# Optimization experiments

Measured on AMD Instinct MI355X. Metric: run time of the kernel, lower is better.

## Reference

```python
import jax, jax.numpy as jnp
import numpy as np

NUM_HEADS = 8
NUM_LEVELS = 4
NUM_POINTS = 4
EMBED = 256
HEAD_DIM = EMBED // NUM_HEADS
SPATIAL = [(100, 100), (50, 50), (25, 25), (13, 13)]  # (H, W) per level


def _bilinear_sample(val, grid):
    """torch.nn.functional.grid_sample(mode='bilinear', padding_mode='zeros', align_corners=False).
    val: [B, H, W, C], grid: [B, N, 2] with (x, y) in [-1, 1]. Returns [B, N, C]."""
    B, H, W, C = val.shape
    x = (grid[..., 0] + 1.0) * (W * 0.5) - 0.5
    y = (grid[..., 1] + 1.0) * (H * 0.5) - 0.5
    x0 = jnp.floor(x)
    y0 = jnp.floor(y)
    wx1 = x - x0
    wy1 = y - y0
    wx0 = 1.0 - wx1
    wy0 = 1.0 - wy1
    x0i = x0.astype(jnp.int32)
    y0i = y0.astype(jnp.int32)
    valf = val.reshape(B, H * W, C)

    def corner(xi, yi, w):
        valid = (xi >= 0) & (xi < W) & (yi >= 0) & (yi < H)
        idx = jnp.clip(yi, 0, H - 1) * W + jnp.clip(xi, 0, W - 1)
        v = jnp.take_along_axis(valf, idx[..., None], axis=1)  # [B, N, C]
        return v * (w * valid)[..., None]

    return (corner(x0i, y0i, wx0 * wy0) + corner(x0i + 1, y0i, wx1 * wy0)
            + corner(x0i, y0i + 1, wx0 * wy1) + corner(x0i + 1, y0i + 1, wx1 * wy1))


def setup_inputs() -> dict:
    key = jax.random.key(0)
    ks = jax.random.split(key, 12)
    bs, nq = 4, 6000
    nv = sum(h * w for h, w in SPATIAL)
    s = 0.02
    return {
        "query": jax.random.normal(ks[0], (bs, nq, EMBED), jnp.float32),
        "value": jax.random.normal(ks[1], (bs, nv, EMBED), jnp.float32),
        "reference_points": jax.random.uniform(ks[2], (bs, nq, NUM_LEVELS, 2), jnp.float32),
        "W_off": jax.random.normal(ks[3], (EMBED, NUM_HEADS * NUM_LEVELS * NUM_POINTS * 2), jnp.float32) * s,
        "b_off": jax.random.normal(ks[4], (NUM_HEADS * NUM_LEVELS * NUM_POINTS * 2,), jnp.float32),
        "W_attn": jax.random.normal(ks[5], (EMBED, NUM_HEADS * NUM_LEVELS * NUM_POINTS), jnp.float32) * s,
        "b_attn": jnp.zeros((NUM_HEADS * NUM_LEVELS * NUM_POINTS,), jnp.float32),
        "W_val": jax.random.normal(ks[6], (EMBED, EMBED), jnp.float32) * s,
        "b_val": jnp.zeros((EMBED,), jnp.float32),
        "W_out": jax.random.normal(ks[7], (EMBED, EMBED), jnp.float32) * s,
        "b_out": jnp.zeros((EMBED,), jnp.float32),
        "spatial_shapes": jnp.asarray(np.array(SPATIAL, dtype=np.int32)),
    }


def reference(query, value, reference_points, W_off, b_off, W_attn, b_attn,
              W_val, b_val, W_out, b_out, spatial_shapes):
    shapes = [(int(h), int(w)) for h, w in np.asarray(spatial_shapes)]
    bs, nq, _ = query.shape
    nv = value.shape[1]

    v = (value @ W_val + b_val).reshape(bs, nv, NUM_HEADS, HEAD_DIM)
    offsets = (query @ W_off + b_off).reshape(bs, nq, NUM_HEADS, NUM_LEVELS, NUM_POINTS, 2)
    aw = (query @ W_attn + b_attn).reshape(bs, nq, NUM_HEADS, NUM_LEVELS * NUM_POINTS)
    aw = jax.nn.softmax(aw, axis=-1).reshape(bs, nq, NUM_HEADS, NUM_LEVELS, NUM_POINTS)

    # offset normalizer is [W, H] per level
    norm = jnp.asarray([[w, h] for h, w in shapes], dtype=query.dtype)  # [L, 2]
    loc = reference_points[:, :, None, :, None, :] + offsets / norm[None, None, None, :, None, :]
    grids = 2.0 * loc - 1.0  # [bs, nq, H, L, P, 2]
    # -> [bs*H, nq*P, 2] per level
    grids = jnp.transpose(grids, (0, 2, 1, 3, 4, 5)).reshape(bs * NUM_HEADS, nq, NUM_LEVELS, NUM_POINTS, 2)

    v_bh = jnp.transpose(v, (0, 2, 1, 3)).reshape(bs * NUM_HEADS, nv, HEAD_DIM)
    sampled = []
    start = 0
    for l, (H_, W_) in enumerate(shapes):
        val_l = v_bh[:, start:start + H_ * W_].reshape(bs * NUM_HEADS, H_, W_, HEAD_DIM)
        grid_l = grids[:, :, l].reshape(bs * NUM_HEADS, nq * NUM_POINTS, 2)
        s_l = _bilinear_sample(val_l, grid_l).reshape(bs * NUM_HEADS, nq, NUM_POINTS, HEAD_DIM)
        sampled.append(s_l)
        start += H_ * W_
    sampled = jnp.stack(sampled, axis=2)  # [bs*H, nq, L, P, c]

    aw_bh = jnp.transpose(aw, (0, 2, 1, 3, 4)).reshape(bs * NUM_HEADS, nq, NUM_LEVELS, NUM_POINTS)
    out = (sampled * aw_bh[..., None]).sum(axis=(2, 3))  # [bs*H, nq, c]
    out = out.reshape(bs, NUM_HEADS, nq, HEAD_DIM).transpose(0, 2, 1, 3).reshape(bs, nq, EMBED)
    out = out @ W_out + b_out
    return out + query
```

## Files before the change

kernel.cpp:

```cpp
#include <hip/hip_runtime.h>
#include <hip/hip_bf16.h>

#define BS 4
#define NQ 6000
#define NV 13294
#define NH 8
#define HD 32
#define EMB 256
#define MV (BS * NV)
#define MQ (BS * NQ)

typedef __attribute__((ext_vector_type(8))) short short8;
typedef __attribute__((ext_vector_type(4))) float floatx4;

__device__ __constant__ float LVL_DIM[4] = {100.f, 50.f, 25.f, 13.f};

__device__ inline unsigned short bf16bits(float f) {
  __hip_bfloat16 h = __float2bfloat16(f);
  return *reinterpret_cast<unsigned short*>(&h);
}
__device__ inline float bflo(unsigned int u) { return __uint_as_float(u << 16); }
__device__ inline float bfhi(unsigned int u) { return __uint_as_float(u & 0xffff0000u); }

#define LDSTR 72

__global__ __launch_bounds__(256) void wtrans_kernel(
    const float* __restrict__ W_val, const float* __restrict__ W_off,
    const float* __restrict__ W_attn, const float* __restrict__ W_out,
    unsigned short* __restrict__ Wt_val, unsigned short* __restrict__ Wt_qcat,
    unsigned short* __restrict__ Wt_out) {
  const int b = blockIdx.x, k = threadIdx.x;
  if (b < 256) {
    Wt_val[b * EMB + k] = bf16bits(W_val[k * 256 + b]);
  } else if (b < 640) {
    const int n = b - 256;
    float v = (n < 256) ? W_off[k * 256 + n] : W_attn[k * 128 + (n - 256)];
    Wt_qcat[n * EMB + k] = bf16bits(v);
  } else {
    const int n = b - 640;
    Wt_out[n * EMB + k] = bf16bits(W_out[k * 256 + n]);
  }
}

__device__ inline void loadA_f32(const float* __restrict__ A, int M, int m0,
                                 int k0, int tid, float4 ra[8]) {
  const int r = tid >> 1, half = tid & 1;
  const int row = m0 + r;
  if (row < M) {
    const float* src = A + (size_t)row * EMB + k0 + half * 32;
#pragma unroll
    for (int j = 0; j < 8; ++j) ra[j] = *(const float4*)(src + 4 * j);
  } else {
#pragma unroll
    for (int j = 0; j < 8; ++j) ra[j] = make_float4(0.f, 0.f, 0.f, 0.f);
  }
}
__device__ inline void storeA_lds(unsigned short* lds, int tid,
                                  const float4 ra[8]) {
  const int r = tid >> 1, half = tid & 1;
  unsigned short* dst = lds + r * LDSTR + half * 32;
#pragma unroll
  for (int j = 0; j < 8; ++j) {
    ushort4 u;
    u.x = bf16bits(ra[j].x);
    u.y = bf16bits(ra[j].y);
    u.z = bf16bits(ra[j].z);
    u.w = bf16bits(ra[j].w);
    *(ushort4*)(dst + 4 * j) = u;
  }
}
__device__ inline void loadB_bf16(const unsigned short* __restrict__ B, int M,
                                  int n0, int k0, int tid, uint4 rb[4]) {
  const int r = tid >> 1, half = tid & 1;
  const int row = n0 + r;
  if (row < M) {
    const unsigned short* src = B + (size_t)row * EMB + k0 + half * 32;
#pragma unroll
    for (int j = 0; j < 4; ++j) rb[j] = *(const uint4*)(src + 8 * j);
  } else {
#pragma unroll
    for (int j = 0; j < 4; ++j) rb[j] = make_uint4(0, 0, 0, 0);
  }
}
__device__ inline void storeB_lds(unsigned short* lds, int tid,
                                  const uint4 rb[4]) {
  const int r = tid >> 1, half = tid & 1;
  unsigned short* dst = lds + r * LDSTR + half * 32;
#pragma unroll
  for (int j = 0; j < 4; ++j) *(uint4*)(dst + 8 * j) = rb[j];
}

__device__ inline void mfma_step(const unsigned short* ldsA,
                                 const unsigned short* ldsB, int wm, int wn,
                                 int lane, int ksub, floatx4 acc[4][4]) {
  const unsigned short* ap =
      ldsA + (wm * 64 + (lane & 15)) * LDSTR + ksub + (lane >> 4) * 8;
  const unsigned short* bp =
      ldsB + (wn * 64 + (lane & 15)) * LDSTR + ksub + (lane >> 4) * 8;
  short8 af[4], bfr[4];
#pragma unroll
  for (int t = 0; t < 4; ++t) {
    af[t] = *(const short8*)(ap + t * 16 * LDSTR);
    bfr[t] = *(const short8*)(bp + t * 16 * LDSTR);
  }
#pragma unroll
  for (int mt = 0; mt < 4; ++mt)
#pragma unroll
    for (int nt = 0; nt < 4; ++nt)
      acc[mt][nt] = __builtin_amdgcn_mfma_f32_16x16x32_bf16(af[mt], bfr[nt],
                                                            acc[mt][nt], 0, 0, 0);
}

__device__ inline void gemm_loop_f32A(const float* __restrict__ A, int M,
                                      int m0, const unsigned short* __restrict__ B,
                                      int NB, int n0, unsigned short* ldsA,
                                      unsigned short* ldsB, int tid, int wm,
                                      int wn, int lane, floatx4 acc[4][4]) {
  float4 ra[8];
  uint4 rb[4];
  loadA_f32(A, M, m0, 0, tid, ra);
  loadB_bf16(B, NB, n0, 0, tid, rb);
#pragma unroll
  for (int k = 0; k < 4; ++k) {
    storeA_lds(ldsA, tid, ra);
    storeB_lds(ldsB, tid, rb);
    __syncthreads();
    if (k < 3) {
      loadA_f32(A, M, m0, (k + 1) * 64, tid, ra);
      loadB_bf16(B, NB, n0, (k + 1) * 64, tid, rb);
    }
    mfma_step(ldsA, ldsB, wm, wn, lane, 0, acc);
    mfma_step(ldsA, ldsB, wm, wn, lane, 32, acc);
    __syncthreads();
  }
}

__device__ inline void gemm_loop_bf16A(const unsigned short* __restrict__ A,
                                       int M, int m0,
                                       const unsigned short* __restrict__ B,
                                       int NB, int n0, unsigned short* ldsA,
                                       unsigned short* ldsB, int tid, int wm,
                                       int wn, int lane, floatx4 acc[4][4]) {
  uint4 ra[4], rb[4];
  loadB_bf16(A, M, m0, 0, tid, ra);
  loadB_bf16(B, NB, n0, 0, tid, rb);
#pragma unroll
  for (int k = 0; k < 4; ++k) {
    storeB_lds(ldsA, tid, ra);
    storeB_lds(ldsB, tid, rb);
    __syncthreads();
    if (k < 3) {
      loadB_bf16(A, M, m0, (k + 1) * 64, tid, ra);
      loadB_bf16(B, NB, n0, (k + 1) * 64, tid, rb);
    }
    mfma_step(ldsA, ldsB, wm, wn, lane, 0, acc);
    mfma_step(ldsA, ldsB, wm, wn, lane, 32, acc);
    __syncthreads();
  }
}

__global__ __launch_bounds__(256, 2) void vqproj_kernel(
    const float* __restrict__ value, const unsigned short* __restrict__ Wt_val,
    const float* __restrict__ b_val, unsigned short* __restrict__ vbh,
    const float* __restrict__ query, const unsigned short* __restrict__ Wt_qcat,
    const float* __restrict__ refpts, const float* __restrict__ b_off,
    const float* __restrict__ b_attn, float* __restrict__ locbuf,
    float* __restrict__ awbuf) {
  __shared__ unsigned short ldsA[128 * LDSTR];
  __shared__ unsigned short ldsB[128 * LDSTR];
  const int tid = threadIdx.x, lane = tid & 63, w = tid >> 6;
  const int wm = w >> 1, wn = w & 1;
  floatx4 acc[4][4];
  const floatx4 zero = {0.f, 0.f, 0.f, 0.f};
#pragma unroll
  for (int i2 = 0; i2 < 4; i2++)
#pragma unroll
    for (int j = 0; j < 4; j++) acc[i2][j] = zero;
  const int quad = lane >> 4, cl = lane & 15;

  if (blockIdx.x < 832) {
    const int chunk = blockIdx.x >> 4, i = blockIdx.x & 15;
    const int m0 = (chunk * 8 + (i & 7)) * 128;
    const int n0 = (i >> 3) * 128;
    gemm_loop_f32A(value, MV, m0, Wt_val, 256, n0, ldsA, ldsB, tid, wm, wn,
                   lane, acc);
#pragma unroll
    for (int mt = 0; mt < 4; ++mt) {
#pragma unroll
      for (int r = 0; r < 4; ++r) {
        const int row = m0 + wm * 64 + mt * 16 + quad * 4 + r;
        if (row < MV) {
          const int b = row / NV, n = row - b * NV;
#pragma unroll
          for (int nt = 0; nt < 4; ++nt) {
            const int c = n0 + wn * 64 + nt * 16 + cl;
            const int h = c >> 5, d = c & 31;
            vbh[(((size_t)(b * NH + h)) * NV + n) * HD + d] =
                bf16bits(acc[mt][nt][r] + b_val[c]);
          }
        }
      }
    }
  } else {
    const int bid = blockIdx.x - 832;
    const int chunk = bid / 24, i = bid % 24;
    const int m_idx = chunk * 8 + (i & 7);
    if (m_idx >= 188) return;
    const int m0 = m_idx * 128;
    const int n0 = (i >> 3) * 128;
    gemm_loop_f32A(query, MQ, m0, Wt_qcat, 384, n0, ldsA, ldsB, tid, wm, wn,
                   lane, acc);
    if (n0 < 256) {
#pragma unroll
      for (int mt = 0; mt < 4; ++mt) {
#pragma unroll
        for (int r = 0; r < 4; ++r) {
          const int row = m0 + wm * 64 + mt * 16 + quad * 4 + r;
          if (row < MQ) {
#pragma unroll
            for (int nt = 0; nt < 4; ++nt) {
              const int c = n0 + wn * 64 + nt * 16 + cl;
              const int xy = c & 1, l = (c >> 3) & 3;
              const float dim = LVL_DIM[l];
              const float ref = refpts[(size_t)row * 8 + l * 2 + xy];
              locbuf[(size_t)row * 256 + c] =
                  ref * dim + acc[mt][nt][r] + b_off[c] - 0.5f;
            }
          }
        }
      }
    } else {
#pragma unroll
      for (int mt = 0; mt < 4; ++mt) {
#pragma unroll
        for (int r = 0; r < 4; ++r) {
          const int row = m0 + wm * 64 + mt * 16 + quad * 4 + r;
          if (row < MQ) {
#pragma unroll
            for (int nt = 0; nt < 4; ++nt) {
              const int ca = wn * 64 + nt * 16 + cl;
              float v = acc[mt][nt][r] + b_attn[ca];
              float m = v;
              m = fmaxf(m, __shfl_xor(m, 1));
              m = fmaxf(m, __shfl_xor(m, 2));
              m = fmaxf(m, __shfl_xor(m, 4));
              m = fmaxf(m, __shfl_xor(m, 8));
              float e = __expf(v - m);
              float s = e;
              s += __shfl_xor(s, 1);
              s += __shfl_xor(s, 2);
              s += __shfl_xor(s, 4);
              s += __shfl_xor(s, 8);
              awbuf[(size_t)row * 128 + ca] = e / s;
            }
          }
        }
      }
    }
  }
}

__global__ __launch_bounds__(256, 4) void sample_kernel(
    const unsigned short* __restrict__ vbh, const float* __restrict__ locbuf,
    const float* __restrict__ awbuf, unsigned short* __restrict__ sampledb) {
  const int blk = blockIdx.x;
  const int t = blk >> 3;
  const int quarter = t / 750;
  const int j = t - quarter * 750;
  const int slice = (blk & 7) * 4 + quarter;
  const int h = slice & 7;
  const int w = threadIdx.x >> 6;
  const int lane = threadIdx.x & 63;
  const int r0 = (slice >> 3) * NQ + j * 8 + w * 2;
  const int g = lane >> 2;
  const int d8 = lane & 3;
  const int l = g >> 2;

  const int W_ = (l < 2) ? ((l == 0) ? 100 : 50) : ((l == 2) ? 25 : 13);
  const int START = (l < 2) ? ((l == 0) ? 0 : 10000) : ((l == 2) ? 12500 : 13125);
  const unsigned int* base =
      (const unsigned int*)vbh + ((size_t)slice * NV + START) * 16 + d8 * 4;

  float acc0[8], acc1[8];
#pragma unroll
  for (int rr = 0; rr < 2; ++rr) {
    const int row = r0 + rr;
    float* a = rr ? acc1 : acc0;
    const float2 xy =
        *(const float2*)(locbuf + (size_t)row * 256 + h * 32 + g * 2);
    const float wgt = awbuf[(size_t)row * 128 + h * 16 + g];

    const float fx = floorf(xy.x), fy = floorf(xy.y);
    const int x0 = (int)fx, y0 = (int)fy;
    const float wx1 = xy.x - fx, wy1 = xy.y - fy;
    const float wx0 = 1.f - wx1, wy0 = 1.f - wy1;
    const int x0c = min(max(x0, 0), W_ - 1), x1c = min(max(x0 + 1, 0), W_ - 1);
    const int y0c = min(max(y0, 0), W_ - 1), y1c = min(max(y0 + 1, 0), W_ - 1);
    const float mx0 = ((unsigned)x0 < (unsigned)W_) ? wx0 : 0.f;
    const float mx1 = ((unsigned)(x0 + 1) < (unsigned)W_) ? wx1 : 0.f;
    const float my0 = ((unsigned)y0 < (unsigned)W_) ? wy0 : 0.f;
    const float my1 = ((unsigned)(y0 + 1) < (unsigned)W_) ? wy1 : 0.f;
    const float wy0w = wgt * my0, wy1w = wgt * my1;
    const float w00 = wy0w * mx0, w01 = wy0w * mx1;
    const float w10 = wy1w * mx0, w11 = wy1w * mx1;

    const int rb0 = y0c * W_, rb1 = y1c * W_;
    const uint4 u00 = *(const uint4*)(base + (size_t)(rb0 + x0c) * 16);
    const uint4 u01 = *(const uint4*)(base + (size_t)(rb0 + x1c) * 16);
    const uint4 u10 = *(const uint4*)(base + (size_t)(rb1 + x0c) * 16);
    const uint4 u11 = *(const uint4*)(base + (size_t)(rb1 + x1c) * 16);
    const unsigned int* p00 = &u00.x;
    const unsigned int* p01 = &u01.x;
    const unsigned int* p10 = &u10.x;
    const unsigned int* p11 = &u11.x;
#pragma unroll
    for (int k = 0; k < 4; ++k) {
      a[2 * k] = w00 * bflo(p00[k]) + w01 * bflo(p01[k]) + w10 * bflo(p10[k]) +
                 w11 * bflo(p11[k]);
      a[2 * k + 1] = w00 * bfhi(p00[k]) + w01 * bfhi(p01[k]) +
                     w10 * bfhi(p10[k]) + w11 * bfhi(p11[k]);
    }
  }

  const bool b0 = (lane >> 2) & 1;
  const bool b1 = (lane >> 3) & 1;
  const bool b2 = (lane >> 4) & 1;
#pragma unroll
  for (int rr = 0; rr < 2; ++rr) {
    float* v = rr ? acc1 : acc0;
#pragma unroll
    for (int jj = 0; jj < 4; ++jj) {
      float lo = v[jj], hi = v[jj + 4];
      float recv = __shfl_xor(b0 ? lo : hi, 4);
      v[jj] = (b0 ? hi : lo) + recv;
    }
#pragma unroll
    for (int jj = 0; jj < 2; ++jj) {
      float lo = v[jj], hi = v[jj + 2];
      float recv = __shfl_xor(b1 ? lo : hi, 8);
      v[jj] = (b1 ? hi : lo) + recv;
    }
    {
      float lo = v[0], hi = v[1];
      float recv = __shfl_xor(b2 ? lo : hi, 16);
      v[0] = (b2 ? hi : lo) + recv;
    }
    v[0] += __shfl_xor(v[0], 32);
  }

  const int dim = d8 * 8 + (b0 ? 4 : 0) + (b1 ? 2 : 0) + (b2 ? 1 : 0);
  const int row = (lane < 32) ? r0 : (r0 + 1);
  const float val = (lane < 32) ? acc0[0] : acc1[0];
  sampledb[(size_t)row * EMB + h * 32 + dim] = bf16bits(val);
}

__global__ __launch_bounds__(256, 2) void oproj_kernel(
    const unsigned short* __restrict__ sampledb,
    const unsigned short* __restrict__ Wt, const float* __restrict__ b_out,
    const float* __restrict__ query, float* __restrict__ out) {
  __shared__ unsigned short ldsA[128 * LDSTR];
  __shared__ unsigned short ldsB[128 * LDSTR];
  const int tid = threadIdx.x, lane = tid & 63, w = tid >> 6;
  const int wm = w >> 1, wn = w & 1;
  const int chunk = blockIdx.x >> 4, i = blockIdx.x & 15;
  const int m_idx = chunk * 8 + (i & 7);
  if (m_idx >= 188) return;
  const int m0 = m_idx * 128;
  const int n0 = (i >> 3) * 128;
  floatx4 acc[4][4];
  const floatx4 zero = {0.f, 0.f, 0.f, 0.f};
#pragma unroll
  for (int i2 = 0; i2 < 4; i2++)
#pragma unroll
    for (int j = 0; j < 4; j++) acc[i2][j] = zero;

  gemm_loop_bf16A(sampledb, MQ, m0, Wt, 256, n0, ldsA, ldsB, tid, wm, wn, lane,
                  acc);

  const int quad = lane >> 4, cl = lane & 15;
#pragma unroll
  for (int mt = 0; mt < 4; ++mt) {
#pragma unroll
    for (int r = 0; r < 4; ++r) {
      const int row = m0 + wm * 64 + mt * 16 + quad * 4 + r;
      if (row < MQ) {
#pragma unroll
        for (int nt = 0; nt < 4; ++nt) {
          const int c = n0 + wn * 64 + nt * 16 + cl;
          out[(size_t)row * EMB + c] =
              acc[mt][nt][r] + b_out[c] + query[(size_t)row * EMB + c];
        }
      }
    }
  }
}

extern "C" void kernel_launch(void* const* d_in, const int* in_sizes, int n_in,
                              void* d_out, int out_size, void* d_ws,
                              size_t ws_size, hipStream_t stream) {
  const float* query  = (const float*)d_in[0];
  const float* value  = (const float*)d_in[1];
  const float* refpts = (const float*)d_in[2];
  const float* W_off  = (const float*)d_in[3];
  const float* b_off  = (const float*)d_in[4];
  const float* W_attn = (const float*)d_in[5];
  const float* b_attn = (const float*)d_in[6];
  const float* W_val  = (const float*)d_in[7];
  const float* b_val  = (const float*)d_in[8];
  const float* W_out  = (const float*)d_in[9];
  const float* b_out  = (const float*)d_in[10];
  float* out = (float*)d_out;

  char* ws = (char*)d_ws;
  unsigned short* vbh = (unsigned short*)ws;
  float* locbuf = (float*)(ws + 27226112);
  float* awbuf = (float*)(ws + 51802112);
  unsigned short* sampledb = (unsigned short*)(ws + 64090112);
  unsigned short* Wt_val = (unsigned short*)(ws + 76378112);
  unsigned short* Wt_qcat = (unsigned short*)(ws + 76509184);
  unsigned short* Wt_out = (unsigned short*)(ws + 76705792);

  wtrans_kernel<<<896, 256, 0, stream>>>(W_val, W_off, W_attn, W_out, Wt_val,
                                         Wt_qcat, Wt_out);
  vqproj_kernel<<<1408, 256, 0, stream>>>(value, Wt_val, b_val, vbh, query,
                                          Wt_qcat, refpts, b_off, b_attn,
                                          locbuf, awbuf);
  sample_kernel<<<24000, 256, 0, stream>>>(vbh, locbuf, awbuf, sampledb);
  oproj_kernel<<<384, 256, 0, stream>>>(sampledb, Wt_out, b_out, query, out);
}
```

Measured before the change: 247.7 us.

## Keep full weight tile resident in LDS and stream A directly into registers

```diff
diff --git a/kernel.cpp b/kernel.cpp
--- a/kernel.cpp
+++ b/kernel.cpp
@@ -22,7 +22,18 @@
 __device__ inline float bflo(unsigned int u) { return __uint_as_float(u << 16); }
 __device__ inline float bfhi(unsigned int u) { return __uint_as_float(u & 0xffff0000u); }
 
-#define LDSTR 72
+__device__ inline short8 cvt8(float4 a, float4 b) {
+  short8 r;
+  r[0] = (short)bf16bits(a.x);
+  r[1] = (short)bf16bits(a.y);
+  r[2] = (short)bf16bits(a.z);
+  r[3] = (short)bf16bits(a.w);
+  r[4] = (short)bf16bits(b.x);
+  r[5] = (short)bf16bits(b.y);
+  r[6] = (short)bf16bits(b.z);
+  r[7] = (short)bf16bits(b.w);
+  return r;
+}
 
 __global__ __launch_bounds__(256) void wtrans_kernel(
     const float* __restrict__ W_val, const float* __restrict__ W_off,
@@ -42,120 +53,119 @@
   }
 }
 
-__device__ inline void loadA_f32(const float* __restrict__ A, int M, int m0,
-                                 int k0, int tid, float4 ra[8]) {
-  const int r = tid >> 1, half = tid & 1;
-  const int row = m0 + r;
-  if (row < M) {
-    const float* src = A + (size_t)row * EMB + k0 + half * 32;
-#pragma unroll
-    for (int j = 0; j < 8; ++j) ra[j] = *(const float4*)(src + 4 * j);
+__device__ inline void loadB_tile(const unsigned short* __restrict__ B, int NB,
+                                  int n0, unsigned short* ldsB, int tid) {
+  const int n = tid >> 1, h = tid & 1;
+  const int row = n0 + n;
+  unsigned short* dst = ldsB + n * 256;
+  if (row < NB) {
+    const unsigned short* src = B + (size_t)row * EMB;
+#pragma unroll
+    for (int j = 0; j < 16; ++j) {
+      const int g = h * 16 + j;
+      *(uint4*)(dst + (((g ^ (n & 31)) << 3))) =
+          *(const uint4*)(src + (g << 3));
+    }
   } else {
-#pragma unroll
-    for (int j = 0; j < 8; ++j) ra[j] = make_float4(0.f, 0.f, 0.f, 0.f);
-  }
-}
-__device__ inline void storeA_lds(unsigned short* lds, int tid,
-                                  const float4 ra[8]) {
-  const int r = tid >> 1, half = tid & 1;
-  unsigned short* dst = lds + r * LDSTR + half * 32;
-#pragma unroll
-  for (int j = 0; j < 8; ++j) {
-    ushort4 u;
-    u.x = bf16bits(ra[j].x);
-    u.y = bf16bits(ra[j].y);
-    u.z = bf16bits(ra[j].z);
-    u.w = bf16bits(ra[j].w);
-    *(ushort4*)(dst + 4 * j) = u;
-  }
-}
-__device__ inline void loadB_bf16(const unsigned short* __restrict__ B, int M,
-                                  int n0, int k0, int tid, uint4 rb[4]) {
-  const int r = tid >> 1, half = tid & 1;
-  const int row = n0 + r;
-  if (row < M) {
-    const unsigned short* src = B + (size_t)row * EMB + k0 + half * 32;
-#pragma unroll
-    for (int j = 0; j < 4; ++j) rb[j] = *(const uint4*)(src + 8 * j);
-  } else {
-#pragma unroll
-    for (int j = 0; j < 4; ++j) rb[j] = make_uint4(0, 0, 0, 0);
-  }
-}
-__device__ inline void storeB_lds(unsigned short* lds, int tid,
-                                  const uint4 rb[4]) {
-  const int r = tid >> 1, half = tid & 1;
-  unsigned short* dst = lds + r * LDSTR + half * 32;
-#pragma unroll
-  for (int j = 0; j < 4; ++j) *(uint4*)(dst + 8 * j) = rb[j];
-}
-
-__device__ inline void mfma_step(const unsigned short* ldsA,
-                                 const unsigned short* ldsB, int wm, int wn,
-                                 int lane, int ksub, floatx4 acc[4][4]) {
-  const unsigned short* ap =
-      ldsA + (wm * 64 + (lane & 15)) * LDSTR + ksub + (lane >> 4) * 8;
-  const unsigned short* bp =
-      ldsB + (wn * 64 + (lane & 15)) * LDSTR + ksub + (lane >> 4) * 8;
-  short8 af[4], bfr[4];
-#pragma unroll
-  for (int t = 0; t < 4; ++t) {
-    af[t] = *(const short8*)(ap + t * 16 * LDSTR);
-    bfr[t] = *(const short8*)(bp + t * 16 * LDSTR);
-  }
-#pragma unroll
-  for (int mt = 0; mt < 4; ++mt)
-#pragma unroll
-    for (int nt = 0; nt < 4; ++nt)
-      acc[mt][nt] = __builtin_amdgcn_mfma_f32_16x16x32_bf16(af[mt], bfr[nt],
-                                                            acc[mt][nt], 0, 0, 0);
-}
-
-__device__ inline void gemm_loop_f32A(const float* __restrict__ A, int M,
-                                      int m0, const unsigned short* __restrict__ B,
-                                      int NB, int n0, unsigned short* ldsA,
-                                      unsigned short* ldsB, int tid, int wm,
-                                      int wn, int lane, floatx4 acc[4][4]) {
-  float4 ra[8];
-  uint4 rb[4];
-  loadA_f32(A, M, m0, 0, tid, ra);
-  loadB_bf16(B, NB, n0, 0, tid, rb);
-#pragma unroll
-  for (int k = 0; k < 4; ++k) {
-    storeA_lds(ldsA, tid, ra);
-    storeB_lds(ldsB, tid, rb);
-    __syncthreads();
-    if (k < 3) {
-      loadA_f32(A, M, m0, (k + 1) * 64, tid, ra);
-      loadB_bf16(B, NB, n0, (k + 1) * 64, tid, rb);
-    }
-    mfma_step(ldsA, ldsB, wm, wn, lane, 0, acc);
-    mfma_step(ldsA, ldsB, wm, wn, lane, 32, acc);
-    __syncthreads();
-  }
-}
-
-__device__ inline void gemm_loop_bf16A(const unsigned short* __restrict__ A,
+    uint4 z = make_uint4(0, 0, 0, 0);
+#pragma unroll
+    for (int j = 0; j < 16; ++j) {
+      const int g = h * 16 + j;
+      *(uint4*)(dst + (((g ^ (n & 31)) << 3))) = z;
+    }
+  }
+}
+
+__device__ inline void gemm_bres_f32A(const float* __restrict__ A, int M,
+                                      int m0, const unsigned short* ldsB,
+                                      int wm, int wn, int lane,
+                                      floatx4 acc[4][4]) {
+  const int quad = lane >> 4, ml = lane & 15;
+  const float* aptr[4];
+#pragma unroll
+  for (int mt = 0; mt < 4; ++mt) {
+    int row = m0 + wm * 64 + mt * 16 + ml;
+    row = min(row, M - 1);
+    aptr[mt] = A + (size_t)row * EMB + quad * 8;
+  }
+  float4 fa[2][8];
+#pragma unroll
+  for (int p = 0; p < 2; ++p)
+#pragma unroll
+    for (int mt = 0; mt < 4; ++mt) {
+      fa[p][2 * mt] = *(const float4*)(aptr[mt] + p * 32);
+      fa[p][2 * mt + 1] = *(const float4*)(aptr[mt] + p * 32 + 4);
+    }
+#pragma unroll
+  for (int k = 0; k < 8; ++k) {
+    short8 af[4];
+#pragma unroll
+    for (int mt = 0; mt < 4; ++mt)
+      af[mt] = cvt8(fa[k & 1][2 * mt], fa[k & 1][2 * mt + 1]);
+    if (k + 2 < 8) {
+#pragma unroll
+      for (int mt = 0; mt < 4; ++mt) {
+        fa[k & 1][2 * mt] = *(const float4*)(aptr[mt] + (k + 2) * 32);
+        fa[k & 1][2 * mt + 1] = *(const float4*)(aptr[mt] + (k + 2) * 32 + 4);
+      }
+    }
+    short8 bf[4];
+#pragma unroll
+    for (int nt = 0; nt < 4; ++nt) {
+      const int n = wn * 64 + nt * 16 + ml;
+      bf[nt] = *(const short8*)(ldsB + n * 256 +
+                                ((((k * 4 + quad) ^ (n & 31)) << 3)));
+    }
+#pragma unroll
+    for (int mt = 0; mt < 4; ++mt)
+#pragma unroll
+      for (int nt = 0; nt < 4; ++nt)
+        acc[mt][nt] = __builtin_amdgcn_mfma_f32_16x16x32_bf16(
+            af[mt], bf[nt], acc[mt][nt], 0, 0, 0);
+  }
+}
+
+__device__ inline void gemm_bres_bf16A(const unsigned short* __restrict__ A,
                                        int M, int m0,
-                                       const unsigned short* __restrict__ B,
-                                       int NB, int n0, unsigned short* ldsA,
-                                       unsigned short* ldsB, int tid, int wm,
+                                       const unsigned short* ldsB, int wm,
                                        int wn, int lane, floatx4 acc[4][4]) {
-  uint4 ra[4], rb[4];
-  loadB_bf16(A, M, m0, 0, tid, ra);
-  loadB_bf16(B, NB, n0, 0, tid, rb);
-#pragma unroll
-  for (int k = 0; k < 4; ++k) {
-    storeB_lds(ldsA, tid, ra);
-    storeB_lds(ldsB, tid, rb);
-    __syncthreads();
-    if (k < 3) {
-      loadB_bf16(A, M, m0, (k + 1) * 64, tid, ra);
-      loadB_bf16(B, NB, n0, (k + 1) * 64, tid, rb);
-    }
-    mfma_step(ldsA, ldsB, wm, wn, lane, 0, acc);
-    mfma_step(ldsA, ldsB, wm, wn, lane, 32, acc);
-    __syncthreads();
+  const int quad = lane >> 4, ml = lane & 15;
+  const unsigned short* aptr[4];
+#pragma unroll
+  for (int mt = 0; mt < 4; ++mt) {
+    int row = m0 + wm * 64 + mt * 16 + ml;
+    row = min(row, M - 1);
+    aptr[mt] = A + (size_t)row * EMB + quad * 8;
+  }
+  short8 fa[2][4];
+#pragma unroll
+  for (int p = 0; p < 2; ++p)
+#pragma unroll
+    for (int mt = 0; mt < 4; ++mt)
+      fa[p][mt] = *(const short8*)(aptr[mt] + p * 32);
+#pragma unroll
+  for (int k = 0; k < 8; ++k) {
+    short8 af[4];
+#pragma unroll
+    for (int mt = 0; mt < 4; ++mt) af[mt] = fa[k & 1][mt];
+    if (k + 2 < 8) {
+#pragma unroll
+      for (int mt = 0; mt < 4; ++mt)
+        fa[k & 1][mt] = *(const short8*)(aptr[mt] + (k + 2) * 32);
+    }
+    short8 bf[4];
+#pragma unroll
+    for (int nt = 0; nt < 4; ++nt) {
+      const int n = wn * 64 + nt * 16 + ml;
+      bf[nt] = *(const short8*)(ldsB + n * 256 +
+                                ((((k * 4 + quad) ^ (n & 31)) << 3)));
+    }
+#pragma unroll
+    for (int mt = 0; mt < 4; ++mt)
+#pragma unroll
+      for (int nt = 0; nt < 4; ++nt)
+        acc[mt][nt] = __builtin_amdgcn_mfma_f32_16x16x32_bf16(
+            af[mt], bf[nt], acc[mt][nt], 0, 0, 0);
   }
 }
 
@@ -166,8 +176,7 @@
     const float* __restrict__ refpts, const float* __restrict__ b_off,
     const float* __restrict__ b_attn, float* __restrict__ locbuf,
     float* __restrict__ awbuf) {
-  __shared__ unsigned short ldsA[128 * LDSTR];
-  __shared__ unsigned short ldsB[128 * LDSTR];
+  __shared__ unsigned short ldsB[128 * 256];
   const int tid = threadIdx.x, lane = tid & 63, w = tid >> 6;
   const int wm = w >> 1, wn = w & 1;
   floatx4 acc[4][4];
@@ -182,8 +191,9 @@
     const int chunk = blockIdx.x >> 4, i = blockIdx.x & 15;
     const int m0 = (chunk * 8 + (i & 7)) * 128;
     const int n0 = (i >> 3) * 128;
-    gemm_loop_f32A(value, MV, m0, Wt_val, 256, n0, ldsA, ldsB, tid, wm, wn,
-                   lane, acc);
+    loadB_tile(Wt_val, 256, n0, ldsB, tid);
+    __syncthreads();
+    gemm_bres_f32A(value, MV, m0, ldsB, wm, wn, lane, acc);
 #pragma unroll
     for (int mt = 0; mt < 4; ++mt) {
 #pragma unroll
@@ -208,8 +218,9 @@
     if (m_idx >= 188) return;
     const int m0 = m_idx * 128;
     const int n0 = (i >> 3) * 128;
-    gemm_loop_f32A(query, MQ, m0, Wt_qcat, 384, n0, ldsA, ldsB, tid, wm, wn,
-                   lane, acc);
+    loadB_tile(Wt_qcat, 384, n0, ldsB, tid);
+    __syncthreads();
+    gemm_bres_f32A(query, MQ, m0, ldsB, wm, wn, lane, acc);
     if (n0 < 256) {
 #pragma unroll
       for (int mt = 0; mt < 4; ++mt) {
@@ -358,8 +369,7 @@
     const unsigned short* __restrict__ sampledb,
     const unsigned short* __restrict__ Wt, const float* __restrict__ b_out,
     const float* __restrict__ query, float* __restrict__ out) {
-  __shared__ unsigned short ldsA[128 * LDSTR];
-  __shared__ unsigned short ldsB[128 * LDSTR];
+  __shared__ unsigned short ldsB[128 * 256];
   const int tid = threadIdx.x, lane = tid & 63, w = tid >> 6;
   const int wm = w >> 1, wn = w & 1;
   const int chunk = blockIdx.x >> 4, i = blockIdx.x & 15;
@@ -374,8 +384,9 @@
 #pragma unroll
     for (int j = 0; j < 4; j++) acc[i2][j] = zero;
 
-  gemm_loop_bf16A(sampledb, MQ, m0, Wt, 256, n0, ldsA, ldsB, tid, wm, wn, lane,
-                  acc);
+  loadB_tile(Wt, 256, n0, ldsB, tid);
+  __syncthreads();
+  gemm_bres_bf16A(sampledb, MQ, m0, ldsB, wm, wn, lane, acc);
 
   const int quad = lane >> 4, cl = lane & 15;
 #pragma unroll
```

After: 262.7 us. 6.1% more time.
